# Kernel optimization log

Measured on AMD Instinct MI355X. Metric: run time of the kernel, lower is better.

## Reference

```python
import jax, jax.numpy as jnp
import numpy as np

B, NORM_NC, LABEL_NC, STYLE_SIZE, NHIDDEN, H, W, KS = 8, 256, 19, 512, 128, 128, 128, 3
EPS = 1e-5


def conv2d(x, w, b):
    # NCHW conv, stride 1, SAME padding (pw = ks//2)
    y = jax.lax.conv_general_dilated(x, w, window_strides=(1, 1), padding='SAME',
                                     dimension_numbers=('NCHW', 'OIHW', 'NCHW'))
    return y + b[None, :, None, None]


def setup_inputs() -> dict:
    key = jax.random.key(0)
    ks = jax.random.split(key, 16)
    s = 0.05
    return {
        'x': jax.random.normal(ks[0], (B, NORM_NC, H, W), jnp.float32),
        'segmap': jax.random.uniform(ks[1], (B, LABEL_NC, H, W), jnp.float32),
        'style': jax.random.normal(ks[2], (B, LABEL_NC, STYLE_SIZE), jnp.float32),
        'w_shared': jax.random.normal(ks[3], (NHIDDEN, LABEL_NC, KS, KS), jnp.float32) * s,
        'b_shared': jnp.zeros((NHIDDEN,), jnp.float32),
        'w_gamma': jax.random.normal(ks[4], (NORM_NC, NHIDDEN, KS, KS), jnp.float32) * s,
        'b_gamma': jnp.zeros((NORM_NC,), jnp.float32),
        'w_beta': jax.random.normal(ks[5], (NORM_NC, NHIDDEN, KS, KS), jnp.float32) * s,
        'b_beta': jnp.zeros((NORM_NC,), jnp.float32),
        'w_sgamma': jax.random.normal(ks[6], (NORM_NC, STYLE_SIZE, KS, KS), jnp.float32) * s,
        'b_sgamma': jnp.zeros((NORM_NC,), jnp.float32),
        'w_sbeta': jax.random.normal(ks[7], (NORM_NC, STYLE_SIZE, KS, KS), jnp.float32) * s,
        'b_sbeta': jnp.zeros((NORM_NC,), jnp.float32),
        'alpha_beta': jax.random.uniform(ks[8], (1,), jnp.float32),
        'alpha_gamma': jax.random.uniform(ks[9], (1,), jnp.float32),
    }


def reference(x, segmap, style, w_shared, b_shared, w_gamma, b_gamma, w_beta, b_beta,
              w_sgamma, b_sgamma, w_sbeta, b_sbeta, alpha_beta, alpha_gamma):
    # InstanceNorm2d (affine=False): per-(b,c) normalization over HxW, biased var
    mean = jnp.mean(x, axis=(2, 3), keepdims=True)
    var = jnp.var(x, axis=(2, 3), keepdims=True)
    normalized = (x - mean) * jax.lax.rsqrt(var + EPS)

    # segmap already at fm_size == out_size -> nearest interpolate is identity
    actv = jax.nn.relu(conv2d(segmap, w_shared, b_shared))  # (B, nhidden, H, W)

    # fused per-pixel contraction over label channels:
    # (style[b,l,s] * segmap[b,l,h,w]).sum(l) -> (B, style_size, H, W)
    style_map = jnp.einsum('bls,blhw->bshw', style, segmap)

    gamma = conv2d(actv, w_gamma, b_gamma)
    beta = conv2d(actv, w_beta, b_beta)
    gamma_style = conv2d(style_map, w_sgamma, b_sgamma)
    beta_style = conv2d(style_map, w_sbeta, b_sbeta)

    wb = jax.nn.sigmoid(alpha_beta)[0]
    wg = jax.nn.sigmoid(alpha_gamma)[0]
    combined_offset = wb * beta_style + (1.0 - wb) * beta
    combined_scale = wg * gamma_style + (1.0 - wg) * gamma + 1.0
    return normalized * combined_scale + combined_offset
```

## Files before the change

kernel.cpp:

```cpp
#include <hip/hip_runtime.h>
#include <hip/hip_bf16.h>
#include <cstdint>

#define B_ 8
#define LABEL_NC 19
#define H_ 128
#define W_ 128
#define UC 640
#define EPS_ 1e-5f

typedef __attribute__((ext_vector_type(8))) short s8v;
typedef __attribute__((ext_vector_type(4))) float f4v;
typedef __attribute__((ext_vector_type(4))) int i4v;
typedef unsigned short ushort_t;

__device__ __forceinline__ ushort_t f2b(float f) {
    union { float f; uint32_t u; } a; a.f = f;
    uint32_t u = a.u;
    return (ushort_t)((u + 0x7FFFu + ((u >> 16) & 1u)) >> 16);
}

__device__ __forceinline__ void gl2lds16(const ushort_t* g, ushort_t* l) {
    __builtin_amdgcn_global_load_lds(
        (const __attribute__((address_space(1))) unsigned int*)g,
        (__attribute__((address_space(3))) unsigned int*)l, 16, 0, 0);
}

__global__ void __launch_bounds__(256) k_prep(
    const float* __restrict__ w_gamma, const float* __restrict__ w_beta,
    const float* __restrict__ w_sgamma, const float* __restrict__ w_sbeta,
    const float* __restrict__ b_gamma, const float* __restrict__ b_beta,
    const float* __restrict__ b_sgamma, const float* __restrict__ b_sbeta,
    const float* __restrict__ alpha_beta, const float* __restrict__ alpha_gamma,
    ushort_t* __restrict__ Wt, float* __restrict__ bias_s, float* __restrict__ bias_o,
    float* __restrict__ zpage)
{
    float wb = 1.f / (1.f + __expf(-alpha_beta[0]));
    float wg = 1.f / (1.f + __expf(-alpha_gamma[0]));
    int gid = blockIdx.x * 256 + threadIdx.x;
    if (gid < 256) bias_s[gid] = wg * b_sgamma[gid] + (1.f - wg) * b_gamma[gid];
    else if (gid < 512) bias_o[gid - 256] = wb * b_sbeta[gid - 256] + (1.f - wb) * b_beta[gid - 256];
    if (gid < 8192) zpage[gid] = 0.f;

    const int total = 9 * 512 * 640;
    for (int idx = gid; idx < total; idx += gridDim.x * 256) {
        int tap = idx / (512 * 640);
        int r = idx - tap * (512 * 640);
        int co = r / 640, ci = r - co * 640;
        int kh = tap / 3, kw = tap - kh * 3;
        float v;
        if (co < 256) {
            if (ci < 128) v = (1.f - wg) * w_gamma[((co * 128 + ci) * 3 + kh) * 3 + kw];
            else          v = wg * w_sgamma[((co * 512 + (ci - 128)) * 3 + kh) * 3 + kw];
        } else {
            int c2 = co - 256;
            if (ci < 128) v = (1.f - wb) * w_beta[((c2 * 128 + ci) * 3 + kh) * 3 + kw];
            else          v = wb * w_sbeta[((c2 * 512 + (ci - 128)) * 3 + kh) * 3 + kw];
        }
        Wt[idx] = f2b(v);
    }
}

__global__ void __launch_bounds__(256) k_stats(const float* __restrict__ x,
                                               float* __restrict__ mean, float* __restrict__ rstd)
{
    int bc = blockIdx.x;
    const float4* p = (const float4*)(x + (size_t)bc * (H_ * W_));
    float s = 0.f, s2 = 0.f;
    for (int i = threadIdx.x; i < H_ * W_ / 4; i += 256) {
        float4 v = p[i];
        s += v.x + v.y + v.z + v.w;
        s2 += v.x * v.x + v.y * v.y + v.z * v.z + v.w * v.w;
    }
    #pragma unroll
    for (int o = 32; o > 0; o >>= 1) { s += __shfl_xor(s, o); s2 += __shfl_xor(s2, o); }
    __shared__ float red[8];
    int wave = threadIdx.x >> 6, lane = threadIdx.x & 63;
    if (lane == 0) { red[wave] = s; red[wave + 4] = s2; }
    __syncthreads();
    if (threadIdx.x == 0) {
        float ts = red[0] + red[1] + red[2] + red[3];
        float t2 = red[4] + red[5] + red[6] + red[7];
        float m = ts * (1.f / 16384.f);
        float v = t2 * (1.f / 16384.f) - m * m;
        mean[bc] = m;
        rstd[bc] = rsqrtf(v + EPS_);
    }
}

__global__ void __launch_bounds__(256) k_buildU(
    const float* __restrict__ segmap, const float* __restrict__ style,
    const float* __restrict__ w_shared, const float* __restrict__ b_shared,
    ushort_t* __restrict__ U)
{
    int bh = blockIdx.x;
    int b = bh >> 7, h = bh & 127;
    __shared__ float seg[3][LABEL_NC][W_];
    const float* segb = segmap + (size_t)b * (LABEL_NC * H_ * W_);
    for (int idx = threadIdx.x; idx < 3 * LABEL_NC * W_; idx += 256) {
        int w = idx & 127;
        int l = (idx >> 7) % LABEL_NC;
        int rr = idx / (LABEL_NC * W_);
        int hh = h + rr - 1;
        seg[rr][l][w] = (hh >= 0 && hh < H_) ? segb[((size_t)l * H_ + hh) * W_ + w] : 0.f;
    }
    __syncthreads();

    int t = threadIdx.x;
    int w = t & 127;
    int grp = __builtin_amdgcn_readfirstlane(t >> 7);
    ushort_t* Urow = U + (((size_t)(b * H_ + h)) * W_ + w) * UC;

    for (int cb = 0; cb < 4; ++cb) {
        int co0 = grp * 64 + cb * 16;
        float acc[16];
        #pragma unroll
        for (int i = 0; i < 16; ++i) acc[i] = b_shared[co0 + i];
        for (int l = 0; l < LABEL_NC; ++l) {
            #pragma unroll
            for (int kh = 0; kh < 3; ++kh) {
                float sm = (w > 0)   ? seg[kh][l][w - 1] : 0.f;
                float s0 = seg[kh][l][w];
                float sp = (w < 127) ? seg[kh][l][w + 1] : 0.f;
                const float* wp = w_shared + ((size_t)co0 * LABEL_NC + l) * 9 + kh * 3;
                #pragma unroll
                for (int i = 0; i < 16; ++i) {
                    const float* wpi = wp + i * (LABEL_NC * 9);
                    acc[i] += sm * wpi[0] + s0 * wpi[1] + sp * wpi[2];
                }
            }
        }
        #pragma unroll
        for (int i = 0; i < 16; ++i)
            Urow[co0 + i] = f2b(acc[i] > 0.f ? acc[i] : 0.f);
    }

    float segr[LABEL_NC];
    #pragma unroll
    for (int l = 0; l < LABEL_NC; ++l) segr[l] = seg[1][l][w];
    const float* styb = style + (size_t)b * (LABEL_NC * 512);
    for (int sb = 0; sb < 16; ++sb) {
        int s0 = grp * 256 + sb * 16;
        float acc[16];
        #pragma unroll
        for (int i = 0; i < 16; ++i) acc[i] = 0.f;
        for (int l = 0; l < LABEL_NC; ++l) {
            const float* sp = styb + l * 512 + s0;
            float sl = segr[l];
            #pragma unroll
            for (int i = 0; i < 16; ++i) acc[i] += sl * sp[i];
        }
        #pragma unroll
        for (int i = 0; i < 16; ++i) Urow[128 + s0 + i] = f2b(acc[i]);
    }
}

#define BK 32

__global__ void __launch_bounds__(512, 1) k_conv(
    const ushort_t* __restrict__ U, const ushort_t* __restrict__ Wt,
    const ushort_t* __restrict__ zp,
    const float* __restrict__ x, const float* __restrict__ mean, const float* __restrict__ rstd,
    const float* __restrict__ bias_s, const float* __restrict__ bias_o,
    float* __restrict__ out)
{
    int orig = blockIdx.x;
    int wg = (orig & 7) * 128 + (orig >> 3);
    int mtile = wg >> 1;
    int cohalf = wg & 1;
    int b = mtile >> 6;
    int h0 = (mtile & 63) << 1;

    extern __shared__ ushort_t smem[];

    int t = threadIdx.x;
    int wv = t >> 6, ln = t & 63;
    int wm = wv >> 1, wn = wv & 1;

    const ushort_t* Ub = U + (size_t)b * (H_ * W_ * UC);

    f4v acc[4][8] = {};

    auto stage_A = [&](int ci0, int ab) {
        ushort_t* sAb = smem + ab * 16384;
        #pragma unroll
        for (int i = 0; i < 4; ++i) {
            int issue = wv * 4 + i;
            int hh = h0 - 1 + (issue >> 3);
            int w = issue * 16 + (ln >> 2);
            int sl = (ln & 3) ^ (w & 3);
            const ushort_t* src = (hh >= 0 && hh < H_)
                ? Ub + ((size_t)hh * W_ + (w & 127)) * UC + ci0 + (sl << 3)
                : zp + (size_t)ln * 8;
            gl2lds16(src, sAb + (size_t)issue * 512);
        }
    };
    auto stage_B = [&](int tapX, int ci0X, int bi) {
        ushort_t* base = smem + 32768 + bi * 8192;
        #pragma unroll
        for (int j = 0; j < 2; ++j) {
            int issue = wv * 2 + j;
            int c = issue * 16 + (ln >> 2);
            int sl = (ln & 3) ^ (c & 3);
            int gq = (c >> 6) & 1;
            int cbase = ((c >> 7) << 6) + (c & 63);
            int co = gq * 256 + cohalf * 128 + cbase;
            const ushort_t* src = Wt + ((size_t)tapX * 512 + co) * UC + ci0X + (sl << 3);
            gl2lds16(src, base + (size_t)issue * 512);
        }
    };

    stage_A(0, 0);
    stage_B(0, 0, 0);
    stage_B(1, 0, 1);

    int ch = 0, tap = 0, bi = 0;
    for (int g = 0; g < 180; ++g) {
        int dhp1 = tap / 3;
        int dw = tap - dhp1 * 3 - 1;

        if (g == 179)      { asm volatile("s_waitcnt vmcnt(0)" ::: "memory"); }
        else if (tap == 8) { asm volatile("s_waitcnt vmcnt(6)" ::: "memory"); }
        else               { asm volatile("s_waitcnt vmcnt(2)" ::: "memory"); }
        __builtin_amdgcn_s_barrier();

        if (g + 2 < 180) {
            int tap2 = tap + 2, ch2 = ch;
            if (tap2 >= 9) { tap2 -= 9; ++ch2; }
            int bi2 = bi + 2; if (bi2 >= 3) bi2 -= 3;
            stage_B(tap2, ch2 * BK, bi2);
        }
        if (tap == 7 && ch < 19) stage_A((ch + 1) * BK, (ch + 1) & 1);

        ushort_t* sAb = smem + (ch & 1) * 16384;
        ushort_t* sBb = smem + 32768 + bi * 8192;
        int sd = ln >> 4;
        s8v af[4];
        #pragma unroll
        for (int mi = 0; mi < 4; ++mi) {
            int p = wm * 64 + mi * 16 + (ln & 15);
            int r = (p >> 7) + dhp1;
            int q = (p & 127) + dw;
            int qc = q < 0 ? 0 : (q > 127 ? 127 : q);
            s8v v = *(const s8v*)&sAb[(size_t)(((r * 128 + qc) << 2) + (sd ^ (qc & 3))) * 8];
            if (q < 0 || q > 127) { s8v z = {}; v = z; }
            af[mi] = v;
        }
        s8v bf[8];
        #pragma unroll
        for (int ni = 0; ni < 8; ++ni) {
            int c = wn * 128 + (ni >> 2) * 64 + (ni & 3) * 16 + (ln & 15);
            bf[ni] = *(const s8v*)&sBb[(size_t)((c << 2) + (sd ^ (c & 3))) * 8];
        }
        #pragma unroll
        for (int mi = 0; mi < 4; ++mi)
            #pragma unroll
            for (int ni = 0; ni < 8; ++ni)
                acc[mi][ni] = __builtin_amdgcn_mfma_f32_16x16x32_bf16(
                    af[mi], bf[ni], acc[mi][ni], 0, 0, 0);

        if (++tap >= 9) { tap = 0; ++ch; }
        if (++bi >= 3) bi = 0;
    }

    int bc_base = b * 256;
    #pragma unroll
    for (int ni = 0; ni < 4; ++ni) {
        int chn = cohalf * 128 + wn * 64 + ni * 16 + (ln & 15);
        float bs = bias_s[chn] + 1.f;
        float bo = bias_o[chn];
        float mu = mean[bc_base + chn];
        float rs = rstd[bc_base + chn];
        #pragma unroll
        for (int mi = 0; mi < 4; ++mi) {
            #pragma unroll
            for (int r = 0; r < 4; ++r) {
                int p = wm * 64 + mi * 16 + ((ln >> 4) << 2) + r;
                int hh = h0 + (p >> 7);
                int ww = p & 127;
                size_t xi = (((size_t)(bc_base + chn)) * H_ + hh) * W_ + ww;
                float xn = (x[xi] - mu) * rs;
                out[xi] = xn * (acc[mi][ni][r] + bs) + (acc[mi][ni + 4][r] + bo);
            }
        }
    }
}

extern "C" void kernel_launch(void* const* d_in, const int* in_sizes, int n_in,
                              void* d_out, int out_size, void* d_ws, size_t ws_size,
                              hipStream_t stream)
{
    const float* x        = (const float*)d_in[0];
    const float* segmap   = (const float*)d_in[1];
    const float* style    = (const float*)d_in[2];
    const float* w_shared = (const float*)d_in[3];
    const float* b_shared = (const float*)d_in[4];
    const float* w_gamma  = (const float*)d_in[5];
    const float* b_gamma  = (const float*)d_in[6];
    const float* w_beta   = (const float*)d_in[7];
    const float* b_beta   = (const float*)d_in[8];
    const float* w_sgamma = (const float*)d_in[9];
    const float* b_sgamma = (const float*)d_in[10];
    const float* w_sbeta  = (const float*)d_in[11];
    const float* b_sbeta  = (const float*)d_in[12];
    const float* alpha_beta  = (const float*)d_in[13];
    const float* alpha_gamma = (const float*)d_in[14];
    float* out = (float*)d_out;

    char* ws = (char*)d_ws;
    float*    ws_mean  = (float*)(ws + 0);
    float*    ws_rstd  = (float*)(ws + 8192);
    float*    ws_bs    = (float*)(ws + 16384);
    float*    ws_bo    = (float*)(ws + 18432);
    ushort_t* ws_Wt    = (ushort_t*)(ws + 20480);
    ushort_t* ws_zp    = (ushort_t*)(ws + 6 * 1024 * 1024 - 65536);
    ushort_t* ws_U     = (ushort_t*)(ws + 6 * 1024 * 1024);

    (void)hipFuncSetAttribute((const void*)k_conv,
                              hipFuncAttributeMaxDynamicSharedMemorySize, 114688);

    k_prep<<<dim3(2048), dim3(256), 0, stream>>>(w_gamma, w_beta, w_sgamma, w_sbeta,
                                                 b_gamma, b_beta, b_sgamma, b_sbeta,
                                                 alpha_beta, alpha_gamma, ws_Wt, ws_bs, ws_bo,
                                                 (float*)ws_zp);
    k_stats<<<dim3(2048), dim3(256), 0, stream>>>(x, ws_mean, ws_rstd);
    k_buildU<<<dim3(1024), dim3(256), 0, stream>>>(segmap, style, w_shared, b_shared, ws_U);
    k_conv<<<dim3(1024), dim3(512), 114688, stream>>>(ws_U, ws_Wt, ws_zp, x, ws_mean, ws_rstd,
                                                      ws_bs, ws_bo, out);
}
```

Before: 1.094 ms.

## Unroll tap loop in implicit-GEMM conv, change LDS swizzle, raise MFMA priority

Restructures the flat 180-iteration loop into a 20-channel-chunk outer loop with a fully unrolled 9-tap inner loop. Tap indices, buffer indices and wait counts become compile-time constants, which removes per-iteration divisions and branch logic. The LDS XOR swizzle now uses bits 1-2 of the row index instead of bits 0-1, aiming to reduce bank conflicts on the 16-byte reads. The MFMA block is wrapped in s_setprio to favour the matrix work, at the cost of more code size and register pressure from the unrolling.

```diff
diff --git a/kernel.cpp b/kernel.cpp
--- a/kernel.cpp
+++ b/kernel.cpp
@@ -188,7 +188,7 @@
             int issue = wv * 4 + i;
             int hh = h0 - 1 + (issue >> 3);
             int w = issue * 16 + (ln >> 2);
-            int sl = (ln & 3) ^ (w & 3);
+            int sl = (ln & 3) ^ ((w >> 1) & 3);
             const ushort_t* src = (hh >= 0 && hh < H_)
                 ? Ub + ((size_t)hh * W_ + (w & 127)) * UC + ci0 + (sl << 3)
                 : zp + (size_t)ln * 8;
@@ -201,7 +201,7 @@
         for (int j = 0; j < 2; ++j) {
             int issue = wv * 2 + j;
             int c = issue * 16 + (ln >> 2);
-            int sl = (ln & 3) ^ (c & 3);
+            int sl = (ln & 3) ^ ((c >> 1) & 3);
             int gq = (c >> 6) & 1;
             int cbase = ((c >> 7) << 6) + (c & 63);
             int co = gq * 256 + cohalf * 128 + cbase;
@@ -214,53 +214,57 @@
     stage_B(0, 0, 0);
     stage_B(1, 0, 1);
 
-    int ch = 0, tap = 0, bi = 0;
-    for (int g = 0; g < 180; ++g) {
-        int dhp1 = tap / 3;
-        int dw = tap - dhp1 * 3 - 1;
-
-        if (g == 179)      { asm volatile("s_waitcnt vmcnt(0)" ::: "memory"); }
-        else if (tap == 8) { asm volatile("s_waitcnt vmcnt(6)" ::: "memory"); }
-        else               { asm volatile("s_waitcnt vmcnt(2)" ::: "memory"); }
-        __builtin_amdgcn_s_barrier();
-
-        if (g + 2 < 180) {
-            int tap2 = tap + 2, ch2 = ch;
-            if (tap2 >= 9) { tap2 -= 9; ++ch2; }
-            int bi2 = bi + 2; if (bi2 >= 3) bi2 -= 3;
-            stage_B(tap2, ch2 * BK, bi2);
-        }
-        if (tap == 7 && ch < 19) stage_A((ch + 1) * BK, (ch + 1) & 1);
-
+    for (int ch = 0; ch < 20; ++ch) {
+        int ci0 = ch * BK;
         ushort_t* sAb = smem + (ch & 1) * 16384;
-        ushort_t* sBb = smem + 32768 + bi * 8192;
-        int sd = ln >> 4;
-        s8v af[4];
-        #pragma unroll
-        for (int mi = 0; mi < 4; ++mi) {
-            int p = wm * 64 + mi * 16 + (ln & 15);
-            int r = (p >> 7) + dhp1;
-            int q = (p & 127) + dw;
-            int qc = q < 0 ? 0 : (q > 127 ? 127 : q);
-            s8v v = *(const s8v*)&sAb[(size_t)(((r * 128 + qc) << 2) + (sd ^ (qc & 3))) * 8];
-            if (q < 0 || q > 127) { s8v z = {}; v = z; }
-            af[mi] = v;
-        }
-        s8v bf[8];
-        #pragma unroll
-        for (int ni = 0; ni < 8; ++ni) {
-            int c = wn * 128 + (ni >> 2) * 64 + (ni & 3) * 16 + (ln & 15);
-            bf[ni] = *(const s8v*)&sBb[(size_t)((c << 2) + (sd ^ (c & 3))) * 8];
-        }
-        #pragma unroll
-        for (int mi = 0; mi < 4; ++mi)
-            #pragma unroll
-            for (int ni = 0; ni < 8; ++ni)
-                acc[mi][ni] = __builtin_amdgcn_mfma_f32_16x16x32_bf16(
-                    af[mi], bf[ni], acc[mi][ni], 0, 0, 0);
-
-        if (++tap >= 9) { tap = 0; ++ch; }
-        if (++bi >= 3) bi = 0;
+        bool lastch = (ch == 19);
+        #pragma unroll
+        for (int tap = 0; tap < 9; ++tap) {
+            const int dhp1 = tap / 3;
+            const int dw = tap - dhp1 * 3 - 1;
+            const int bi = tap % 3;
+            const int bi2 = (tap + 2) % 3;
+
+            if (tap == 8) {
+                if (lastch) { asm volatile("s_waitcnt vmcnt(0)" ::: "memory"); }
+                else        { asm volatile("s_waitcnt vmcnt(6)" ::: "memory"); }
+            } else          { asm volatile("s_waitcnt vmcnt(2)" ::: "memory"); }
+            __builtin_amdgcn_s_barrier();
+
+            if (tap < 7)        stage_B(tap + 2, ci0, bi2);
+            else if (!lastch) {
+                if (tap == 7) { stage_B(0, ci0 + BK, bi2); stage_A(ci0 + BK, (ch + 1) & 1); }
+                else          stage_B(1, ci0 + BK, bi2);
+            }
+
+            ushort_t* sBb = smem + 32768 + bi * 8192;
+            int sd = ln >> 4;
+            s8v af[4];
+            #pragma unroll
+            for (int mi = 0; mi < 4; ++mi) {
+                int p = wm * 64 + mi * 16 + (ln & 15);
+                int q = (p & 127) + dw;
+                int qc = q < 0 ? 0 : (q > 127 ? 127 : q);
+                int r = (p >> 7) + dhp1;
+                s8v v = *(const s8v*)&sAb[(size_t)(((r * 128 + qc) << 2) + (sd ^ ((qc >> 1) & 3))) * 8];
+                if (dw != 0 && (q < 0 || q > 127)) { s8v z = {}; v = z; }
+                af[mi] = v;
+            }
+            s8v bf[8];
+            #pragma unroll
+            for (int ni = 0; ni < 8; ++ni) {
+                int c = wn * 128 + (ni >> 2) * 64 + (ni & 3) * 16 + (ln & 15);
+                bf[ni] = *(const s8v*)&sBb[(size_t)((c << 2) + (sd ^ ((c >> 1) & 3))) * 8];
+            }
+            __builtin_amdgcn_s_setprio(1);
+            #pragma unroll
+            for (int mi = 0; mi < 4; ++mi)
+                #pragma unroll
+                for (int ni = 0; ni < 8; ++ni)
+                    acc[mi][ni] = __builtin_amdgcn_mfma_f32_16x16x32_bf16(
+                        af[mi], bf[ni], acc[mi][ni], 0, 0, 0);
+            __builtin_amdgcn_s_setprio(0);
+        }
     }
 
     int bc_base = b * 256;
```

Measured after the change: 946.5 us. -13.4%, faster.
